# Kernel tuning notes

Hardware: AMD Instinct MI355X
Metric: run time of the kernel (lower is better)

Reference implementation:

```python
import jax, jax.numpy as jnp
import numpy as np

B, N, T = 1, 1024, 2048   # batch, graph nodes, timesteps
E, K = 16384, 32          # edges, causal kernel taps


def setup_inputs() -> dict:
    key = jax.random.key(0)
    k1, k2, k3, k4 = jax.random.split(key, 4)
    x = jax.random.normal(k1, (B, N, T), dtype=jnp.float32)
    # per-edge causal impulse-response kernels (aggregator(g) output)
    kernel = jax.random.normal(k2, (E, K), dtype=jnp.float32) * 0.1
    src = jax.random.randint(k3, (E,), 0, N)
    dst = jax.random.randint(k4, (E,), 0, N)
    return {"x": x, "kernel": kernel, "src": src, "dst": dst}


def reference(x, kernel, src, dst):
    # Block-sparse causal conv over the edge list:
    #   y_e[b, t] = sum_k kernel[e, k] * x[b, src_e, t - k]   (causal)
    #   out[b, n, t] = x[b, n, t] + sum_{e: dst_e = n} y_e[b, t]
    # (residual applied because g.include_index_diag is False)
    xs = x[:, src, :]                      # [B, E, T] gather upstream signals
    rhs = kernel[:, None, ::-1]            # [E, 1, K] flipped -> true causal conv
    y = jax.lax.conv_general_dilated(
        xs, rhs,
        window_strides=(1,),
        padding=[(K - 1, 0)],              # left-pad: strictly causal
        dimension_numbers=("NCW", "OIW", "NCW"),
        feature_group_count=E,             # one independent kernel per edge
    )                                      # [B, E, T]
    agg = jax.ops.segment_sum(jnp.swapaxes(y, 0, 1), dst, num_segments=N)  # [N, B, T]
    return x + jnp.swapaxes(agg, 0, 1)     # [B, N, T]
```

## Files before the change

kernel.cpp:

```cpp
#include <hip/hip_runtime.h>
#include <hip/hip_bf16.h>

#define TT  2048
#define KK  32
#define NN  1024
#define EE  16384
#define CAP 64

typedef short short8 __attribute__((ext_vector_type(8)));
typedef float f32x4 __attribute__((ext_vector_type(4)));

__device__ __forceinline__ short f2bf(float f) {
    __hip_bfloat16 h = __float2bfloat16(f);
    return __builtin_bit_cast(short, h);
}

__global__ __launch_bounds__(256) void zero_cnt_kernel(int* __restrict__ cnt) {
    const int i = blockIdx.x * 256 + threadIdx.x;
    if (i < NN) cnt[i] = 0;
}

template<bool CSR>
__global__ __launch_bounds__(256) void prep_kernel(
    const float* __restrict__ x, short* __restrict__ xbf,
    const int* __restrict__ src, const int* __restrict__ dst,
    int* __restrict__ cnt, unsigned* __restrict__ slots)
{
    const int i = blockIdx.x * 256 + threadIdx.x;
    const float4* x4 = (const float4*)x;
    const float4 a = x4[2 * i], b = x4[2 * i + 1];
    short8 hh;
    hh[0] = f2bf(a.x); hh[1] = f2bf(a.y); hh[2] = f2bf(a.z); hh[3] = f2bf(a.w);
    hh[4] = f2bf(b.x); hh[5] = f2bf(b.y); hh[6] = f2bf(b.z); hh[7] = f2bf(b.w);
    ((short8*)xbf)[i] = hh;
    if (CSR && i < EE) {
        const int d = dst[i];
        const int p = atomicAdd(&cnt[d], 1);
        if (p < CAP) slots[(size_t)d * CAP + p] = ((unsigned)src[i] << 14) | (unsigned)i;
    }
}

template<int MODE>
__global__ __launch_bounds__(256, 8) void lti_main(
    const float* __restrict__ x, const short* __restrict__ xbf,
    const float* __restrict__ kern, const int* __restrict__ src,
    const int* __restrict__ dst, const int* __restrict__ cnt,
    const unsigned* __restrict__ slots, float* __restrict__ out)
{
    const int n   = blockIdx.x;
    const int tid = threadIdx.x;
    const int w   = tid >> 6;
    const int ln  = tid & 63;
    const int c   = ln & 15, g = ln >> 4;
    const int t0  = 512 * w;

    __shared__ __align__(16) short xs_all[4][544];
    __shared__ __align__(16) short kt_all[4][8][72];
    __shared__ int bl[CAP];
    __shared__ int bc;

    short* xs = xs_all[w];
    short (*kt)[72] = kt_all[w];

    short8 z8; z8[0]=0;z8[1]=0;z8[2]=0;z8[3]=0;z8[4]=0;z8[5]=0;z8[6]=0;z8[7]=0;

    {
        short8* kz = (short8*)&kt[0][0];
        kz[ln] = z8;
        if (ln < 8) kz[64 + ln] = z8;
        if (w == 0 && ln < 4) *(short8*)&xs[8 * ln] = z8;
    }

    int L;
    if (MODE == 2) {
        L = cnt[n]; if (L > CAP) L = CAP;
    } else {
        if (tid == 0) bc = 0;
        __syncthreads();
        const int4* d4 = (const int4*)dst;
        #pragma unroll
        for (int it = 0; it < EE / 1024; ++it) {
            const int i4 = tid + 256 * it;
            const int4 d = d4[i4];
            const int eb = 4 * i4;
            if (d.x == n) { int p = atomicAdd(&bc, 1); if (p < CAP) bl[p] = (src[eb    ] << 14) | (eb    ); }
            if (d.y == n) { int p = atomicAdd(&bc, 1); if (p < CAP) bl[p] = (src[eb + 1] << 14) | (eb + 1); }
            if (d.z == n) { int p = atomicAdd(&bc, 1); if (p < CAP) bl[p] = (src[eb + 2] << 14) | (eb + 2); }
            if (d.w == n) { int p = atomicAdd(&bc, 1); if (p < CAP) bl[p] = (src[eb + 3] << 14) | (eb + 3); }
        }
        __syncthreads();
        L = bc; if (L > CAP) L = CAP;
    }

    f32x4 acc0 = {0,0,0,0}, acc1 = {0,0,0,0};
    short8 row0, rowh = z8;
    short tapbf = 0;

    #define FETCH_SLOT(P) ((MODE == 2) ? slots[(size_t)n * CAP + (P)] : (unsigned)bl[P])

    #define LOAD_EXPERT(SV)                                                            \
    {                                                                                  \
        const int e0 = __builtin_amdgcn_readfirstlane((int)((SV) & 16383u));           \
        const int s0 = __builtin_amdgcn_readfirstlane((int)((SV) >> 14));              \
        if (MODE >= 1) {                                                               \
            row0 = *(const short8*)(xbf + (size_t)s0 * TT + t0 + 8 * ln);              \
            if (w && ln < 4)                                                           \
                rowh = *(const short8*)(xbf + (size_t)s0 * TT + t0 - 32 + 8 * ln);     \
        } else {                                                                       \
            const float4* xr = (const float4*)(x + (size_t)s0 * TT + t0);              \
            float4 u = xr[2 * ln], v = xr[2 * ln + 1];                                 \
            row0[0]=f2bf(u.x); row0[1]=f2bf(u.y); row0[2]=f2bf(u.z); row0[3]=f2bf(u.w);\
            row0[4]=f2bf(v.x); row0[5]=f2bf(v.y); row0[6]=f2bf(v.z); row0[7]=f2bf(v.w);\
            if (w && ln < 4) {                                                         \
                u = *(const float4*)(x + (size_t)s0 * TT + t0 - 32 + 8 * ln);          \
                v = *(const float4*)(x + (size_t)s0 * TT + t0 - 28 + 8 * ln);          \
                rowh[0]=f2bf(u.x); rowh[1]=f2bf(u.y); rowh[2]=f2bf(u.z); rowh[3]=f2bf(u.w); \
                rowh[4]=f2bf(v.x); rowh[5]=f2bf(v.y); rowh[6]=f2bf(v.z); rowh[7]=f2bf(v.w); \
            }                                                                          \
        }                                                                              \
        tapbf = 0;                                                                     \
        if (ln < KK) tapbf = f2bf(kern[(size_t)e0 * KK + ln]);                         \
    }

    #define COMMIT_EXPERT()                                                            \
    {                                                                                  \
        *(short8*)&xs[32 + 8 * ln] = row0;                                             \
        if (w && ln < 4) *(short8*)&xs[8 * ln] = rowh;                                 \
        if (ln < KK) {                                                                 \
            _Pragma("unroll")                                                          \
            for (int a2 = 0; a2 < 8; ++a2)                                             \
                kt[a2][((a2 + 1) & 7) + 47 - ln] = tapbf;                              \
        }                                                                              \
    }

    const int a_ = c & 7;
    const int s1 = ((a_ + 1) & 7) + 15 - c + 8 * g;

    if (L > 0) {
        unsigned sv = FETCH_SLOT(0);
        LOAD_EXPERT(sv);
        for (int p = 0; p < L; ++p) {
            COMMIT_EXPERT();
            const bool hn = (p + 1 < L);
            if (hn) { unsigned svn = FETCH_SLOT(p + 1); LOAD_EXPERT(svn); }

            const short8 b1 = *(const short8*)&kt[a_][s1];
            short8 b2 = *(const short8*)&kt[a_][s1 + 16];
            if (g < 2) b2 = z8;

            {
                const short8 a1  = *(const short8*)&xs[16 * c + 8 * g];
                const short8 a2v = *(const short8*)&xs[16 * c + 8 * g + 16];
                acc0 = __builtin_amdgcn_mfma_f32_16x16x32_bf16(a1,  b1, acc0, 0, 0, 0);
                acc0 = __builtin_amdgcn_mfma_f32_16x16x32_bf16(a2v, b2, acc0, 0, 0, 0);
            }
            {
                const short8 a1  = *(const short8*)&xs[256 + 16 * c + 8 * g];
                const short8 a2v = *(const short8*)&xs[256 + 16 * c + 8 * g + 16];
                acc1 = __builtin_amdgcn_mfma_f32_16x16x32_bf16(a1,  b1, acc1, 0, 0, 0);
                acc1 = __builtin_amdgcn_mfma_f32_16x16x32_bf16(a2v, b2, acc1, 0, 0, 0);
            }
        }
    }

    const float* xr  = x   + (size_t)n * TT + t0;
    float*       orw = out + (size_t)n * TT + t0;
    #pragma unroll
    for (int q = 0; q < 4; ++q) {
        const int ta = 64 * g + 16 * q + c;
        orw[ta]       = xr[ta]       + acc0[q];
        orw[256 + ta] = xr[256 + ta] + acc1[q];
    }
    #undef FETCH_SLOT
    #undef LOAD_EXPERT
    #undef COMMIT_EXPERT
}

extern "C" void kernel_launch(void* const* d_in, const int* in_sizes, int n_in,
                              void* d_out, int out_size, void* d_ws, size_t ws_size,
                              hipStream_t stream) {
    const float* x    = (const float*)d_in[0];
    const float* kern = (const float*)d_in[1];
    const int*   src  = (const int*)d_in[2];
    const int*   dst  = (const int*)d_in[3];
    float*       out  = (float*)d_out;

    const size_t CNT_B  = (size_t)NN * 4;
    const size_t SLOT_B = (size_t)NN * CAP * 4;
    const size_t XBF_B  = (size_t)NN * TT * 2;
    char* wsb = (char*)d_ws;
    int*      cnt   = (int*)wsb;
    unsigned* slots = (unsigned*)(wsb + CNT_B);
    short*    xbf   = (short*)(wsb + CNT_B + SLOT_B);

    if (ws_size >= CNT_B + SLOT_B + XBF_B) {
        zero_cnt_kernel<<<dim3(4), dim3(256), 0, stream>>>(cnt);
        prep_kernel<true><<<dim3(NN * TT / 8 / 256), dim3(256), 0, stream>>>(
            x, xbf, src, dst, cnt, slots);
        lti_main<2><<<dim3(NN), dim3(256), 0, stream>>>(
            x, xbf, kern, src, dst, cnt, slots, out);
    } else if (ws_size >= XBF_B) {
        short* xbf2 = (short*)wsb;
        prep_kernel<false><<<dim3(NN * TT / 8 / 256), dim3(256), 0, stream>>>(
            x, xbf2, src, dst, nullptr, nullptr);
        lti_main<1><<<dim3(NN), dim3(256), 0, stream>>>(
            x, xbf2, kern, src, dst, nullptr, nullptr, out);
    } else {
        lti_main<0><<<dim3(NN), dim3(256), 0, stream>>>(
            x, nullptr, kern, src, dst, nullptr, nullptr, out);
    }
}
```

Measured before the change: 40.13 us.

## Fuse into single kernel with in-block edge scan and double-buffered fp32 gathers

Drops the separate count-zeroing, bf16 conversion and CSR-building kernels and launches one kernel that scans the dst list per block and converts gathered fp32 rows to bf16 on the fly. The edge loop becomes two-deep software pipelined with A/B register buffers, so the next edge's global loads overlap the current MFMA work. Tap loads become one float4 per lane instead of scalar loads, and launch bounds drop to 4 blocks per CU to make room for the extra registers. Each block now re-reads the full dst array and reads fp32 rows at twice the bytes of bf16, in exchange for saving three launches and the global bf16 copy.

```diff
diff --git a/kernel.cpp b/kernel.cpp
--- a/kernel.cpp
+++ b/kernel.cpp
@@ -15,37 +15,12 @@
     return __builtin_bit_cast(short, h);
 }
 
-__global__ __launch_bounds__(256) void zero_cnt_kernel(int* __restrict__ cnt) {
-    const int i = blockIdx.x * 256 + threadIdx.x;
-    if (i < NN) cnt[i] = 0;
-}
-
-template<bool CSR>
-__global__ __launch_bounds__(256) void prep_kernel(
-    const float* __restrict__ x, short* __restrict__ xbf,
-    const int* __restrict__ src, const int* __restrict__ dst,
-    int* __restrict__ cnt, unsigned* __restrict__ slots)
-{
-    const int i = blockIdx.x * 256 + threadIdx.x;
-    const float4* x4 = (const float4*)x;
-    const float4 a = x4[2 * i], b = x4[2 * i + 1];
-    short8 hh;
-    hh[0] = f2bf(a.x); hh[1] = f2bf(a.y); hh[2] = f2bf(a.z); hh[3] = f2bf(a.w);
-    hh[4] = f2bf(b.x); hh[5] = f2bf(b.y); hh[6] = f2bf(b.z); hh[7] = f2bf(b.w);
-    ((short8*)xbf)[i] = hh;
-    if (CSR && i < EE) {
-        const int d = dst[i];
-        const int p = atomicAdd(&cnt[d], 1);
-        if (p < CAP) slots[(size_t)d * CAP + p] = ((unsigned)src[i] << 14) | (unsigned)i;
-    }
-}
-
-template<int MODE>
-__global__ __launch_bounds__(256, 8) void lti_main(
-    const float* __restrict__ x, const short* __restrict__ xbf,
-    const float* __restrict__ kern, const int* __restrict__ src,
-    const int* __restrict__ dst, const int* __restrict__ cnt,
-    const unsigned* __restrict__ slots, float* __restrict__ out)
+__global__ __launch_bounds__(256, 4) void lti_kernel(
+    const float* __restrict__ x,
+    const float* __restrict__ kern,
+    const int*   __restrict__ src,
+    const int*   __restrict__ dst,
+    float*       __restrict__ out)
 {
     const int n   = blockIdx.x;
     const int tid = threadIdx.x;
@@ -64,102 +39,102 @@
 
     short8 z8; z8[0]=0;z8[1]=0;z8[2]=0;z8[3]=0;z8[4]=0;z8[5]=0;z8[6]=0;z8[7]=0;
 
+    if (tid == 0) bc = 0;
     {
         short8* kz = (short8*)&kt[0][0];
         kz[ln] = z8;
         if (ln < 8) kz[64 + ln] = z8;
         if (w == 0 && ln < 4) *(short8*)&xs[8 * ln] = z8;
     }
+    __syncthreads();
 
-    int L;
-    if (MODE == 2) {
-        L = cnt[n]; if (L > CAP) L = CAP;
-    } else {
-        if (tid == 0) bc = 0;
-        __syncthreads();
-        const int4* d4 = (const int4*)dst;
-        #pragma unroll
-        for (int it = 0; it < EE / 1024; ++it) {
-            const int i4 = tid + 256 * it;
-            const int4 d = d4[i4];
-            const int eb = 4 * i4;
-            if (d.x == n) { int p = atomicAdd(&bc, 1); if (p < CAP) bl[p] = (src[eb    ] << 14) | (eb    ); }
-            if (d.y == n) { int p = atomicAdd(&bc, 1); if (p < CAP) bl[p] = (src[eb + 1] << 14) | (eb + 1); }
-            if (d.z == n) { int p = atomicAdd(&bc, 1); if (p < CAP) bl[p] = (src[eb + 2] << 14) | (eb + 2); }
-            if (d.w == n) { int p = atomicAdd(&bc, 1); if (p < CAP) bl[p] = (src[eb + 3] << 14) | (eb + 3); }
-        }
-        __syncthreads();
-        L = bc; if (L > CAP) L = CAP;
+    const int4* d4 = (const int4*)dst;
+    #pragma unroll
+    for (int it = 0; it < EE / 1024; ++it) {
+        const int i4 = tid + 256 * it;
+        const int4 d = d4[i4];
+        const int eb = 4 * i4;
+        if (d.x == n) { int p = atomicAdd(&bc, 1); if (p < CAP) bl[p] = (src[eb    ] << 14) | (eb    ); }
+        if (d.y == n) { int p = atomicAdd(&bc, 1); if (p < CAP) bl[p] = (src[eb + 1] << 14) | (eb + 1); }
+        if (d.z == n) { int p = atomicAdd(&bc, 1); if (p < CAP) bl[p] = (src[eb + 2] << 14) | (eb + 2); }
+        if (d.w == n) { int p = atomicAdd(&bc, 1); if (p < CAP) bl[p] = (src[eb + 3] << 14) | (eb + 3); }
     }
+    __syncthreads();
+    int L = bc; if (L > CAP) L = CAP;
 
     f32x4 acc0 = {0,0,0,0}, acc1 = {0,0,0,0};
-    short8 row0, rowh = z8;
-    short tapbf = 0;
+    short8 rowA, rowB, haloA = z8, haloB = z8;
+    float4 tapA = {0,0,0,0}, tapB = {0,0,0,0};
 
-    #define FETCH_SLOT(P) ((MODE == 2) ? slots[(size_t)n * CAP + (P)] : (unsigned)bl[P])
-
-    #define LOAD_EXPERT(SV)                                                            \
+    #define LOAD_EX(S, SV)                                                             \
     {                                                                                  \
         const int e0 = __builtin_amdgcn_readfirstlane((int)((SV) & 16383u));           \
         const int s0 = __builtin_amdgcn_readfirstlane((int)((SV) >> 14));              \
-        if (MODE >= 1) {                                                               \
-            row0 = *(const short8*)(xbf + (size_t)s0 * TT + t0 + 8 * ln);              \
-            if (w && ln < 4)                                                           \
-                rowh = *(const short8*)(xbf + (size_t)s0 * TT + t0 - 32 + 8 * ln);     \
-        } else {                                                                       \
-            const float4* xr = (const float4*)(x + (size_t)s0 * TT + t0);              \
-            float4 u = xr[2 * ln], v = xr[2 * ln + 1];                                 \
-            row0[0]=f2bf(u.x); row0[1]=f2bf(u.y); row0[2]=f2bf(u.z); row0[3]=f2bf(u.w);\
-            row0[4]=f2bf(v.x); row0[5]=f2bf(v.y); row0[6]=f2bf(v.z); row0[7]=f2bf(v.w);\
-            if (w && ln < 4) {                                                         \
-                u = *(const float4*)(x + (size_t)s0 * TT + t0 - 32 + 8 * ln);          \
-                v = *(const float4*)(x + (size_t)s0 * TT + t0 - 28 + 8 * ln);          \
-                rowh[0]=f2bf(u.x); rowh[1]=f2bf(u.y); rowh[2]=f2bf(u.z); rowh[3]=f2bf(u.w); \
-                rowh[4]=f2bf(v.x); rowh[5]=f2bf(v.y); rowh[6]=f2bf(v.z); rowh[7]=f2bf(v.w); \
-            }                                                                          \
+        const float4* xr = (const float4*)(x + (size_t)s0 * TT + t0);                  \
+        float4 u = xr[2 * ln], v = xr[2 * ln + 1];                                     \
+        row##S[0]=f2bf(u.x); row##S[1]=f2bf(u.y); row##S[2]=f2bf(u.z); row##S[3]=f2bf(u.w); \
+        row##S[4]=f2bf(v.x); row##S[5]=f2bf(v.y); row##S[6]=f2bf(v.z); row##S[7]=f2bf(v.w); \
+        if (w && ln < 4) {                                                             \
+            u = *(const float4*)(x + (size_t)s0 * TT + t0 - 32 + 8 * ln);              \
+            v = *(const float4*)(x + (size_t)s0 * TT + t0 - 28 + 8 * ln);              \
+            halo##S[0]=f2bf(u.x); halo##S[1]=f2bf(u.y); halo##S[2]=f2bf(u.z); halo##S[3]=f2bf(u.w); \
+            halo##S[4]=f2bf(v.x); halo##S[5]=f2bf(v.y); halo##S[6]=f2bf(v.z); halo##S[7]=f2bf(v.w); \
         }                                                                              \
-        tapbf = 0;                                                                     \
-        if (ln < KK) tapbf = f2bf(kern[(size_t)e0 * KK + ln]);                         \
+        tap##S = *(const float4*)(kern + (size_t)e0 * KK + 4 * (ln & 7));              \
     }
 
-    #define COMMIT_EXPERT()                                                            \
+    #define COMMIT_EX(S)                                                               \
     {                                                                                  \
-        *(short8*)&xs[32 + 8 * ln] = row0;                                             \
-        if (w && ln < 4) *(short8*)&xs[8 * ln] = rowh;                                 \
-        if (ln < KK) {                                                                 \
-            _Pragma("unroll")                                                          \
-            for (int a2 = 0; a2 < 8; ++a2)                                             \
-                kt[a2][((a2 + 1) & 7) + 47 - ln] = tapbf;                              \
+        *(short8*)&xs[32 + 8 * ln] = row##S;                                           \
+        if (w && ln < 4) *(short8*)&xs[8 * ln] = halo##S;                              \
+        {        \
+            const int a2  = ln >> 3;                                                   \
+            const int pad = (a2 + 1) & 7;                                              \
+            const int mb  = 4 * (ln & 7);                                              \
+            kt[a2][pad + 47 - mb]     = f2bf(tap##S.x);                                \
+            kt[a2][pad + 46 - mb]     = f2bf(tap##S.y);                                \
+            kt[a2][pad + 45 - mb]     = f2bf(tap##S.z);                                \
+            kt[a2][pad + 44 - mb]     = f2bf(tap##S.w);                                \
         }                                                                              \
     }
 
     const int a_ = c & 7;
     const int s1 = ((a_ + 1) & 7) + 15 - c + 8 * g;
 
+    #define COMPUTE()                                                                  \
+    {                                                                                  \
+        const short8 b1 = *(const short8*)&kt[a_][s1];                                 \
+        short8 b2 = *(const short8*)&kt[a_][s1 + 16];                                  \
+        if (g < 2) b2 = z8;                              \
+        {                                                                              \
+            const short8 a1  = *(const short8*)&xs[16 * c + 8 * g];                    \
+            const short8 a2v = *(const short8*)&xs[16 * c + 8 * g + 16];               \
+            acc0 = __builtin_amdgcn_mfma_f32_16x16x32_bf16(a1,  b1, acc0, 0, 0, 0);    \
+            acc0 = __builtin_amdgcn_mfma_f32_16x16x32_bf16(a2v, b2, acc0, 0, 0, 0);    \
+        }                                                                              \
+        {                                                                              \
+            const short8 a1  = *(const short8*)&xs[256 + 16 * c + 8 * g];              \
+            const short8 a2v = *(const short8*)&xs[256 + 16 * c + 8 * g + 16];         \
+            acc1 = __builtin_amdgcn_mfma_f32_16x16x32_bf16(a1,  b1, acc1, 0, 0, 0);    \
+            acc1 = __builtin_amdgcn_mfma_f32_16x16x32_bf16(a2v, b2, acc1, 0, 0, 0);    \
+        }                                                                              \
+    }
+
     if (L > 0) {
-        unsigned sv = FETCH_SLOT(0);
-        LOAD_EXPERT(sv);
-        for (int p = 0; p < L; ++p) {
-            COMMIT_EXPERT();
-            const bool hn = (p + 1 < L);
-            if (hn) { unsigned svn = FETCH_SLOT(p + 1); LOAD_EXPERT(svn); }
+        unsigned svA = (unsigned)bl[0];
+        LOAD_EX(A, svA);
+        COMMIT_EX(A);
+        if (L > 1) { unsigned svB = (unsigned)bl[1]; LOAD_EX(B, svB); }
+        svA = (L > 2) ? (unsigned)bl[2] : 0u;
 
-            const short8 b1 = *(const short8*)&kt[a_][s1];
-            short8 b2 = *(const short8*)&kt[a_][s1 + 16];
-            if (g < 2) b2 = z8;
-
-            {
-                const short8 a1  = *(const short8*)&xs[16 * c + 8 * g];
-                const short8 a2v = *(const short8*)&xs[16 * c + 8 * g + 16];
-                acc0 = __builtin_amdgcn_mfma_f32_16x16x32_bf16(a1,  b1, acc0, 0, 0, 0);
-                acc0 = __builtin_amdgcn_mfma_f32_16x16x32_bf16(a2v, b2, acc0, 0, 0, 0);
-            }
-            {
-                const short8 a1  = *(const short8*)&xs[256 + 16 * c + 8 * g];
-                const short8 a2v = *(const short8*)&xs[256 + 16 * c + 8 * g + 16];
-                acc1 = __builtin_amdgcn_mfma_f32_16x16x32_bf16(a1,  b1, acc1, 0, 0, 0);
-                acc1 = __builtin_amdgcn_mfma_f32_16x16x32_bf16(a2v, b2, acc1, 0, 0, 0);
-            }
+        for (int p = 0; p < L; p += 2) {
+            const unsigned svC = (p + 3 < L) ? (unsigned)bl[p + 3] : 0u;
+            COMPUTE();
+            if (p + 2 < L) LOAD_EX(A, svA);
+            if (p + 1 < L) { COMMIT_EX(B); COMPUTE(); }
+            if (p + 4 < L) svA = (unsigned)bl[p + 4];
+            if (p + 3 < L) LOAD_EX(B, svC);
+            if (p + 2 < L) COMMIT_EX(A);
         }
     }
 
@@ -171,9 +146,9 @@
         orw[ta]       = xr[ta]       + acc0[q];
         orw[256 + ta] = xr[256 + ta] + acc1[q];
     }
-    #undef FETCH_SLOT
-    #undef LOAD_EXPERT
-    #undef COMMIT_EXPERT
+    #undef LOAD_EX
+    #undef COMMIT_EX
+    #undef COMPUTE
 }
 
 extern "C" void kernel_launch(void* const* d_in, const int* in_sizes, int n_in,
@@ -185,28 +160,5 @@
     const int*   dst  = (const int*)d_in[3];
     float*       out  = (float*)d_out;
 
-    const size_t CNT_B  = (size_t)NN * 4;
-    const size_t SLOT_B = (size_t)NN * CAP * 4;
-    const size_t XBF_B  = (size_t)NN * TT * 2;
-    char* wsb = (char*)d_ws;
-    int*      cnt   = (int*)wsb;
-    unsigned* slots = (unsigned*)(wsb + CNT_B);
-    short*    xbf   = (short*)(wsb + CNT_B + SLOT_B);
-
-    if (ws_size >= CNT_B + SLOT_B + XBF_B) {
-        zero_cnt_kernel<<<dim3(4), dim3(256), 0, stream>>>(cnt);
-        prep_kernel<true><<<dim3(NN * TT / 8 / 256), dim3(256), 0, stream>>>(
-            x, xbf, src, dst, cnt, slots);
-        lti_main<2><<<dim3(NN), dim3(256), 0, stream>>>(
-            x, xbf, kern, src, dst, cnt, slots, out);
-    } else if (ws_size >= XBF_B) {
-        short* xbf2 = (short*)wsb;
-        prep_kernel<false><<<dim3(NN * TT / 8 / 256), dim3(256), 0, stream>>>(
-            x, xbf2, src, dst, nullptr, nullptr);
-        lti_main<1><<<dim3(NN), dim3(256), 0, stream>>>(
-            x, xbf2, kern, src, dst, nullptr, nullptr, out);
-    } else {
-        lti_main<0><<<dim3(NN), dim3(256), 0, stream>>>(
-            x, nullptr, kern, src, dst, nullptr, nullptr, out);
-    }
+    lti_kernel<<<dim3(NN), dim3(256), 0, stream>>>(x, kern, src, dst, out);
 }
```

Measured after the change: 42.90 us. +6.9%, slower.
